# Kernel tuning notes

Measured on AMD Instinct MI355X. Metric: run time of the kernel, lower is better.

## Reference

```python
import jax, jax.numpy as jnp
import numpy as np

EPS = 1e-08
TEMPERATURE = 1.0
HEADS = 4
OUT_DIM = 32
IN_DIM = 128
N_NODES = 100000
N_EDGES = 1600000


def setup_inputs() -> dict:
    key = jax.random.key(0)
    k1, k2, k3, k4, k5, k6 = jax.random.split(key, 6)
    x = jax.random.normal(k1, (N_NODES, IN_DIM), dtype=jnp.float32)
    # nn.Linear(in_dim, heads*out_dim, bias=False).weight -> [heads*out_dim, in_dim]
    W = jax.random.normal(k2, (HEADS * OUT_DIM, IN_DIM), dtype=jnp.float32) * 0.05
    a_src = jax.random.normal(k3, (HEADS, OUT_DIM), dtype=jnp.float32) * 0.1
    a_dst = jax.random.normal(k4, (HEADS, OUT_DIM), dtype=jnp.float32) * 0.1
    edge_index = jax.random.randint(k5, (2, N_EDGES), 0, N_NODES, dtype=jnp.int32)
    rnbrw_weights = jax.random.uniform(k6, (N_EDGES,), dtype=jnp.float32)
    return {"x": x, "W": W, "a_src": a_src, "a_dst": a_dst,
            "edge_index": edge_index, "rnbrw_weights": rnbrw_weights}


def reference(x, W, a_src, a_dst, edge_index, rnbrw_weights):
    N = x.shape[0]
    heads, out_dim = a_src.shape
    # h = W(x).view(N, heads, out_dim)
    h = (x @ W.T).reshape(N, heads, out_dim)
    src, dst = edge_index[0], edge_index[1]
    h_src = h[src]  # [E, heads, out_dim]
    h_dst = h[dst]  # [E, heads, out_dim]
    # per-edge attention scores [E, heads]
    score = jnp.einsum('ehd,hd->eh', h_src, a_src) + jnp.einsum('ehd,hd->eh', h_dst, a_dst)
    # strategy == 'pre_softmax_bias'
    score = score + jnp.log(rnbrw_weights + EPS)[:, None]
    score = jnp.where(score >= 0, score, 0.2 * score)  # leaky_relu(0.2)
    scaled = score / TEMPERATURE
    # edge softmax over incoming edges of each dst node
    seg_max = jax.ops.segment_max(scaled, dst, num_segments=N)      # [N, heads]
    exp_s = jnp.exp(scaled - seg_max[dst])                           # [E, heads]
    denom = jax.ops.segment_sum(exp_s, dst, num_segments=N)         # [N, heads]
    alpha = exp_s / (denom[dst] + EPS)                               # [E, heads]
    # scatter-add aggregation: out[dst] += alpha * h_src
    out = jax.ops.segment_sum(alpha[..., None] * h_src, dst, num_segments=N)
    out = out.reshape(N, heads * out_dim)
    return out, alpha
```

## Files before the change

### kernel.cpp

```cpp
#include <hip/hip_runtime.h>

#define EPS 1e-8f

__device__ inline unsigned short f2bf(float f) {
    unsigned u = __float_as_uint(f);
    unsigned r = u + 0x7fffu + ((u >> 16) & 1u);
    return (unsigned short)(r >> 16);
}
__device__ inline float bflo(unsigned v) { return __uint_as_float(v << 16); }
__device__ inline float bfhi(unsigned v) { return __uint_as_float(v & 0xffff0000u); }

__device__ inline float bsel(float4 es4, int i, int head) {
    float x = __shfl(es4.x, i, 32);
    float y = __shfl(es4.y, i, 32);
    float z = __shfl(es4.z, i, 32);
    float w = __shfl(es4.w, i, 32);
    return head == 0 ? x : head == 1 ? y : head == 2 ? z : w;
}

__global__ __launch_bounds__(256) void gemm_s_kernel(
    const float* __restrict__ x, const float* __restrict__ W,
    const float* __restrict__ a_src, const float* __restrict__ a_dst,
    unsigned short* __restrict__ hb, float* __restrict__ s_src, float* __restrict__ s_dst,
    int N, int n_tiles)
{
    __shared__ float Wt[128 * 64];
    __shared__ float xt[128 * 64];

    const int t = threadIdx.x;
    const int half = blockIdx.y;
    const float* Wh = W + half * 64 * 128;

#pragma unroll
    for (int p = 0; p < 8; ++p) {
        int idx = p * 256 + t;
        int ol = (idx & 31) | ((idx >> 10) << 5);
        int k4 = (idx >> 5) & 31;
        float4 w = *(const float4*)(Wh + ol * 128 + k4 * 4);
        Wt[(4 * k4 + 0) * 64 + ol] = w.x;
        Wt[(4 * k4 + 1) * 64 + ol] = w.y;
        Wt[(4 * k4 + 2) * 64 + ol] = w.z;
        Wt[(4 * k4 + 3) * 64 + ol] = w.w;
    }
    __syncthreads();

    const int o4 = t & 15;
    const int n4g = t >> 4;
    const int head = half * 2 + (o4 >> 3);
    const float4 as = *(const float4*)(a_src + head * 32 + (o4 & 7) * 4);
    const float4 ad = *(const float4*)(a_dst + head * 32 + (o4 & 7) * 4);

    for (int tile = blockIdx.x; tile < n_tiles; tile += gridDim.x) {
        const int nbase = tile * 64;
        __syncthreads();
#pragma unroll
        for (int p = 0; p < 8; ++p) {
            int idx = p * 256 + t;
            int n = idx & 63;
            int k4 = idx >> 6;
            int ng = nbase + n;
            float4 v = make_float4(0.f, 0.f, 0.f, 0.f);
            if (ng < N) v = *(const float4*)(x + (size_t)ng * 128 + k4 * 4);
            xt[(4 * k4 + 0) * 64 + n] = v.x;
            xt[(4 * k4 + 1) * 64 + n] = v.y;
            xt[(4 * k4 + 2) * 64 + n] = v.z;
            xt[(4 * k4 + 3) * 64 + n] = v.w;
        }
        __syncthreads();

        float acc[4][4];
#pragma unroll
        for (int i = 0; i < 4; ++i)
#pragma unroll
            for (int j = 0; j < 4; ++j) acc[i][j] = 0.f;

        for (int k = 0; k < 128; ++k) {
            float4 wv = *(const float4*)(Wt + k * 64 + 4 * o4);
            float4 xv = *(const float4*)(xt + k * 64 + 4 * n4g);
            float wa[4] = {wv.x, wv.y, wv.z, wv.w};
            float xa[4] = {xv.x, xv.y, xv.z, xv.w};
#pragma unroll
            for (int i = 0; i < 4; ++i)
#pragma unroll
                for (int j = 0; j < 4; ++j) acc[i][j] += xa[i] * wa[j];
        }

#pragma unroll
        for (int i = 0; i < 4; ++i) {
            int n = nbase + 4 * n4g + i;
            float ps = acc[i][0] * as.x + acc[i][1] * as.y + acc[i][2] * as.z + acc[i][3] * as.w;
            float pd = acc[i][0] * ad.x + acc[i][1] * ad.y + acc[i][2] * ad.z + acc[i][3] * ad.w;
            ps += __shfl_xor(ps, 1); ps += __shfl_xor(ps, 2); ps += __shfl_xor(ps, 4);
            pd += __shfl_xor(pd, 1); pd += __shfl_xor(pd, 2); pd += __shfl_xor(pd, 4);
            if (n < N) {
                ushort4 hv;
                hv.x = f2bf(acc[i][0]); hv.y = f2bf(acc[i][1]);
                hv.z = f2bf(acc[i][2]); hv.w = f2bf(acc[i][3]);
                *(ushort4*)(hb + (size_t)n * 128 + half * 64 + 4 * o4) = hv;
                if ((o4 & 7) == 0) {
                    s_src[n * 4 + head] = ps;
                    s_dst[n * 4 + head] = pd;
                }
            }
        }
    }
}

__global__ __launch_bounds__(256) void edge_score_kernel(
    const int* __restrict__ src, const int* __restrict__ dst,
    const float* __restrict__ rnbrw,
    const float* __restrict__ s_src, const float* __restrict__ s_dst,
    float* __restrict__ es_orig, int* __restrict__ counts, int E)
{
    int e = blockIdx.x * 256 + threadIdx.x;
    if (e >= E) return;
    int s = src[e], d = dst[e];
    float lw = __logf(rnbrw[e] + EPS);
    float4 a = *(const float4*)(s_src + s * 4);
    float4 b = *(const float4*)(s_dst + d * 4);
    float sc[4] = {a.x + b.x + lw, a.y + b.y + lw, a.z + b.z + lw, a.w + b.w + lw};
    float es[4];
#pragma unroll
    for (int hh = 0; hh < 4; ++hh) {
        float v = sc[hh];
        v = (v >= 0.f) ? v : 0.2f * v;
        es[hh] = __expf(v);
    }
    *(float4*)(es_orig + (size_t)e * 4) = make_float4(es[0], es[1], es[2], es[3]);
    atomicAdd(counts + d, 1);
}

__global__ __launch_bounds__(256) void scan1_kernel(
    const int* __restrict__ counts, int* __restrict__ offs, int* __restrict__ bsum, int N)
{
    __shared__ int sh[256];
    int t = threadIdx.x;
    int base = blockIdx.x * 1024 + t * 4;
    int c[4];
#pragma unroll
    for (int j = 0; j < 4; ++j) c[j] = (base + j < N) ? counts[base + j] : 0;
    int tsum = c[0] + c[1] + c[2] + c[3];
    sh[t] = tsum;
    __syncthreads();
    for (int off = 1; off < 256; off <<= 1) {
        int v = (t >= off) ? sh[t - off] : 0;
        __syncthreads();
        sh[t] += v;
        __syncthreads();
    }
    int run = sh[t] - tsum;
    if (t == 255) bsum[blockIdx.x] = sh[255];
#pragma unroll
    for (int j = 0; j < 4; ++j) {
        if (base + j < N) { offs[base + j] = run; run += c[j]; }
    }
}

__global__ void scan2_kernel(int* __restrict__ bsum, int nb)
{
    if (threadIdx.x == 0) {
        int acc = 0;
        for (int i = 0; i < nb; ++i) { int v = bsum[i]; bsum[i] = acc; acc += v; }
    }
}

__global__ __launch_bounds__(256) void scan3_kernel(
    int* __restrict__ offs, const int* __restrict__ bsum,
    int* __restrict__ cursor, int N)
{
    int i = blockIdx.x * 256 + threadIdx.x;
    if (i >= N) return;
    int v = offs[i] + bsum[i >> 10];
    offs[i] = v;
    cursor[i] = v;
}

__global__ __launch_bounds__(256) void scatter_kernel(
    const int* __restrict__ src, const int* __restrict__ dst,
    const float* __restrict__ es_orig, int* __restrict__ cursor,
    int* __restrict__ csr_src, int* __restrict__ csr_eid,
    float* __restrict__ csr_es, int E)
{
    int e = blockIdx.x * 256 + threadIdx.x;
    if (e >= E) return;
    int pos = atomicAdd(cursor + dst[e], 1);
    csr_src[pos] = src[e];
    csr_eid[pos] = e;
    *(float4*)(csr_es + (size_t)pos * 4) = *(const float4*)(es_orig + (size_t)e * 4);
}

__global__ __launch_bounds__(256) void node_aggr_kernel(
    const int* __restrict__ offs, const int* __restrict__ counts,
    const int* __restrict__ csr_src, const int* __restrict__ csr_eid,
    const float* __restrict__ csr_es,
    const unsigned short* __restrict__ hb,
    float* __restrict__ alpha, float* __restrict__ out, int N)
{
    int gid = blockIdx.x * 256 + threadIdx.x;
    int n = gid >> 5;
    int l = gid & 31;
    if (n >= N) return;

    int beg = offs[n];
    int cnt = counts[n];
    int head = l >> 3;

    float4 acc = make_float4(0.f, 0.f, 0.f, 0.f);
    float den = 0.f;

    for (int base = 0; base < cnt; base += 32) {
        int m = cnt - base; if (m > 32) m = 32;
        int sl = 0;
        float4 es4 = make_float4(0.f, 0.f, 0.f, 0.f);
        if (l < m) {
            int p = beg + base + l;
            sl = csr_src[p];
            es4 = *(const float4*)(csr_es + (size_t)p * 4);
        }
        int mr = (m + 3) & ~3;
        for (int i = 0; i < mr; i += 4) {
            int s0 = __shfl(sl, i + 0, 32);
            int s1 = __shfl(sl, i + 1, 32);
            int s2 = __shfl(sl, i + 2, 32);
            int s3 = __shfl(sl, i + 3, 32);
            uint2 v0 = *(const uint2*)(hb + (size_t)s0 * 128 + l * 4);
            uint2 v1 = *(const uint2*)(hb + (size_t)s1 * 128 + l * 4);
            uint2 v2 = *(const uint2*)(hb + (size_t)s2 * 128 + l * 4);
            uint2 v3 = *(const uint2*)(hb + (size_t)s3 * 128 + l * 4);
            float e0 = bsel(es4, i + 0, head);
            float e1 = bsel(es4, i + 1, head);
            float e2 = bsel(es4, i + 2, head);
            float e3 = bsel(es4, i + 3, head);
            acc.x += e0 * bflo(v0.x); acc.y += e0 * bfhi(v0.x);
            acc.z += e0 * bflo(v0.y); acc.w += e0 * bfhi(v0.y);
            acc.x += e1 * bflo(v1.x); acc.y += e1 * bfhi(v1.x);
            acc.z += e1 * bflo(v1.y); acc.w += e1 * bfhi(v1.y);
            acc.x += e2 * bflo(v2.x); acc.y += e2 * bfhi(v2.x);
            acc.z += e2 * bflo(v2.y); acc.w += e2 * bfhi(v2.y);
            acc.x += e3 * bflo(v3.x); acc.y += e3 * bfhi(v3.x);
            acc.z += e3 * bflo(v3.y); acc.w += e3 * bfhi(v3.y);
            den += e0 + e1 + e2 + e3;
        }
    }

    float inv_h[4];
#pragma unroll
    for (int q = 0; q < 4; ++q) {
        float dq = __shfl(den, q << 3, 32);
        inv_h[q] = 1.f / (dq + EPS);
    }

    float inv = inv_h[head];
    acc.x *= inv; acc.y *= inv; acc.z *= inv; acc.w *= inv;
    *(float4*)(out + (size_t)n * 128 + l * 4) = acc;

    for (int base = 0; base < cnt; base += 32) {
        int m = cnt - base; if (m > 32) m = 32;
        if (l < m) {
            int p = beg + base + l;
            int eid = csr_eid[p];
            float4 es4 = *(const float4*)(csr_es + (size_t)p * 4);
            float4 al = make_float4(es4.x * inv_h[0], es4.y * inv_h[1],
                                    es4.z * inv_h[2], es4.w * inv_h[3]);
            *(float4*)(alpha + (size_t)eid * 4) = al;
        }
    }
}

extern "C" void kernel_launch(void* const* d_in, const int* in_sizes, int n_in,
                              void* d_out, int out_size, void* d_ws, size_t ws_size,
                              hipStream_t stream) {
    const float* x      = (const float*)d_in[0];
    const float* W      = (const float*)d_in[1];
    const float* a_src  = (const float*)d_in[2];
    const float* a_dst  = (const float*)d_in[3];
    const int*   eidx   = (const int*)d_in[4];
    const float* rnbrw  = (const float*)d_in[5];

    const int E = in_sizes[5];
    const int N = in_sizes[0] / 128;

    float* out   = (float*)d_out;
    float* alpha = out + (size_t)N * 128;
    float* es_orig = alpha;

    char* w = (char*)d_ws;
    unsigned short* hb = (unsigned short*)w;  w += (size_t)N * 128 * 2;
    float* s_src = (float*)w;                 w += (size_t)N * 4 * 4;
    float* s_dst = (float*)w;                 w += (size_t)N * 4 * 4;
    int* counts  = (int*)w;                   w += (size_t)N * 4;
    int* offs    = (int*)w;                   w += (size_t)N * 4;
    int* cursor  = (int*)w;                   w += (size_t)N * 4;
    int* bsum    = (int*)w;                   w += 512;
    int* csr_src = (int*)w;                   w += (size_t)E * 4;
    int* csr_eid = (int*)w;                   w += (size_t)E * 4;
    float* csr_es = (float*)w;

    const int* src = eidx;
    const int* dst = eidx + E;

    hipMemsetAsync(counts, 0, (size_t)N * sizeof(int), stream);

    int n_tiles = (N + 63) / 64;
    dim3 gridA(512, 2);
    gemm_s_kernel<<<gridA, 256, 0, stream>>>(x, W, a_src, a_dst, hb, s_src, s_dst, N, n_tiles);

    int eblocks = (E + 255) / 256;
    edge_score_kernel<<<eblocks, 256, 0, stream>>>(src, dst, rnbrw, s_src, s_dst,
                                                   es_orig, counts, E);

    int nb = (N + 1023) / 1024;
    scan1_kernel<<<nb, 256, 0, stream>>>(counts, offs, bsum, N);
    scan2_kernel<<<1, 64, 0, stream>>>(bsum, nb);
    scan3_kernel<<<(N + 255) / 256, 256, 0, stream>>>(offs, bsum, cursor, N);

    scatter_kernel<<<eblocks, 256, 0, stream>>>(src, dst, es_orig, cursor,
                                                csr_src, csr_eid, csr_es, E);

    int ablocks = ((size_t)N * 32 + 255) / 256;
    node_aggr_kernel<<<ablocks, 256, 0, stream>>>(offs, counts, csr_src, csr_eid,
                                                  csr_es, hb, alpha, out, N);
}
```

Before: 443.4 us.

## Shrink CSR records and normalize alpha in a separate coalesced edge pass

Measured after the change: 483.3 us. 1.09x slower.

```diff
diff --git a/kernel.cpp b/kernel.cpp
--- a/kernel.cpp
+++ b/kernel.cpp
@@ -177,24 +177,19 @@
 
 __global__ __launch_bounds__(256) void scatter_kernel(
     const int* __restrict__ src, const int* __restrict__ dst,
-    const float* __restrict__ es_orig, int* __restrict__ cursor,
-    int* __restrict__ csr_src, int* __restrict__ csr_eid,
-    float* __restrict__ csr_es, int E)
+    int* __restrict__ cursor, int2* __restrict__ rec, int E)
 {
     int e = blockIdx.x * 256 + threadIdx.x;
     if (e >= E) return;
     int pos = atomicAdd(cursor + dst[e], 1);
-    csr_src[pos] = src[e];
-    csr_eid[pos] = e;
-    *(float4*)(csr_es + (size_t)pos * 4) = *(const float4*)(es_orig + (size_t)e * 4);
+    rec[pos] = make_int2(src[e], e);
 }
 
 __global__ __launch_bounds__(256) void node_aggr_kernel(
     const int* __restrict__ offs, const int* __restrict__ counts,
-    const int* __restrict__ csr_src, const int* __restrict__ csr_eid,
-    const float* __restrict__ csr_es,
+    const int2* __restrict__ rec, const float* __restrict__ es_orig,
     const unsigned short* __restrict__ hb,
-    float* __restrict__ alpha, float* __restrict__ out, int N)
+    float* __restrict__ inv_den, float* __restrict__ out, int N)
 {
     int gid = blockIdx.x * 256 + threadIdx.x;
     int n = gid >> 5;
@@ -213,9 +208,9 @@
         int sl = 0;
         float4 es4 = make_float4(0.f, 0.f, 0.f, 0.f);
         if (l < m) {
-            int p = beg + base + l;
-            sl = csr_src[p];
-            es4 = *(const float4*)(csr_es + (size_t)p * 4);
+            int2 r = rec[(size_t)(beg + base + l)];
+            sl = r.x;
+            es4 = *(const float4*)(es_orig + (size_t)r.y * 4);
         }
         int mr = (m + 3) & ~3;
         for (int i = 0; i < mr; i += 4) {
@@ -254,17 +249,22 @@
     acc.x *= inv; acc.y *= inv; acc.z *= inv; acc.w *= inv;
     *(float4*)(out + (size_t)n * 128 + l * 4) = acc;
 
-    for (int base = 0; base < cnt; base += 32) {
-        int m = cnt - base; if (m > 32) m = 32;
-        if (l < m) {
-            int p = beg + base + l;
-            int eid = csr_eid[p];
-            float4 es4 = *(const float4*)(csr_es + (size_t)p * 4);
-            float4 al = make_float4(es4.x * inv_h[0], es4.y * inv_h[1],
-                                    es4.z * inv_h[2], es4.w * inv_h[3]);
-            *(float4*)(alpha + (size_t)eid * 4) = al;
-        }
-    }
+    if (l == 0)
+        *(float4*)(inv_den + (size_t)n * 4) =
+            make_float4(inv_h[0], inv_h[1], inv_h[2], inv_h[3]);
+}
+
+__global__ __launch_bounds__(256) void alpha_kernel(
+    const int* __restrict__ dst, const float* __restrict__ inv_den,
+    float* __restrict__ alpha, int E)
+{
+    int e = blockIdx.x * 256 + threadIdx.x;
+    if (e >= E) return;
+    int d = dst[e];
+    float4 es = *(const float4*)(alpha + (size_t)e * 4);
+    float4 iv = *(const float4*)(inv_den + (size_t)d * 4);
+    es.x *= iv.x; es.y *= iv.y; es.z *= iv.z; es.w *= iv.w;
+    *(float4*)(alpha + (size_t)e * 4) = es;
 }
 
 extern "C" void kernel_launch(void* const* d_in, const int* in_sizes, int n_in,
@@ -286,15 +286,14 @@
 
     char* w = (char*)d_ws;
     unsigned short* hb = (unsigned short*)w;  w += (size_t)N * 128 * 2;
-    float* s_src = (float*)w;                 w += (size_t)N * 4 * 4;
-    float* s_dst = (float*)w;                 w += (size_t)N * 4 * 4;
     int* counts  = (int*)w;                   w += (size_t)N * 4;
     int* offs    = (int*)w;                   w += (size_t)N * 4;
     int* cursor  = (int*)w;                   w += (size_t)N * 4;
     int* bsum    = (int*)w;                   w += 512;
-    int* csr_src = (int*)w;                   w += (size_t)E * 4;
-    int* csr_eid = (int*)w;                   w += (size_t)E * 4;
-    float* csr_es = (float*)w;
+    float* inv_den = (float*)w;               w += (size_t)N * 4 * 4;
+    int2* rec    = (int2*)w;
+    float* s_src = (float*)w;
+    float* s_dst = s_src + (size_t)N * 4;
 
     const int* src = eidx;
     const int* dst = eidx + E;
@@ -314,10 +313,11 @@
     scan2_kernel<<<1, 64, 0, stream>>>(bsum, nb);
     scan3_kernel<<<(N + 255) / 256, 256, 0, stream>>>(offs, bsum, cursor, N);
 
-    scatter_kernel<<<eblocks, 256, 0, stream>>>(src, dst, es_orig, cursor,
-                                                csr_src, csr_eid, csr_es, E);
+    scatter_kernel<<<eblocks, 256, 0, stream>>>(src, dst, cursor, rec, E);
 
     int ablocks = ((size_t)N * 32 + 255) / 256;
-    node_aggr_kernel<<<ablocks, 256, 0, stream>>>(offs, counts, csr_src, csr_eid,
-                                                  csr_es, hb, alpha, out, N);
-}
+    node_aggr_kernel<<<ablocks, 256, 0, stream>>>(offs, counts, rec, es_orig, hb,
+                                                  inv_den, out, N);
+
+    alpha_kernel<<<eblocks, 256, 0, stream>>>(dst, inv_den, alpha, E);
+}
```
